# Performance work log

Measured on AMD Instinct MI355X. Metric: run time of the kernel, lower is better.

The kernel has to match this reference:

```python
import jax, jax.numpy as jnp
import numpy as np

B, N, C, H, NL, NH = 8, 1024, 256, 512, 3, 8


def setup_inputs() -> dict:
    key = jax.random.key(0)
    ks = jax.random.split(key, 16)
    g = lambda k, shape: jax.random.normal(k, shape, jnp.float32) * 0.02
    return dict(
        concept_features=jax.random.normal(ks[0], (B, N, C), jnp.float32),
        adjacency_matrix=jax.random.uniform(ks[1], (B, N, N), jnp.float32),
        edge_types=jax.random.randint(ks[2], (B, N, N), 0, 10),
        concept_mask=jnp.ones((B, N), bool),
        W_emb=g(ks[3], (H, C)), b_emb=jnp.zeros((H,), jnp.float32),
        W_in=g(ks[4], (NL, 3 * H, H)), b_in=jnp.zeros((NL, 3 * H), jnp.float32),
        W_out=g(ks[5], (NL, H, H)), b_out=jnp.zeros((NL, H), jnp.float32),
        W_conv=g(ks[6], (NL, H, H)), b_conv=jnp.zeros((NL, H), jnp.float32),
        W_cls=g(ks[7], (1, H)), b_cls=jnp.zeros((1,), jnp.float32),
        W_diff=g(ks[8], (5, H)), b_diff=jnp.zeros((5,), jnp.float32),
        W_pre=g(ks[9], (1, 2 * H)), b_pre=jnp.zeros((1,), jnp.float32),
        W_pool=g(ks[10], (H, H)), b_pool=jnp.zeros((H,), jnp.float32),
    )


def reference(concept_features, adjacency_matrix, edge_types, concept_mask,
              W_emb, b_emb, W_in, b_in, W_out, b_out, W_conv, b_conv,
              W_cls, b_cls, W_diff, b_diff, W_pre, b_pre, W_pool, b_pool):
    Bq, Nc, _ = concept_features.shape
    Hd = W_emb.shape[0]
    dh = Hd // NH

    def mha(x, Wi, bi, Wo, bo):
        # torch nn.MultiheadAttention with batch_first=False: the (B,N,H)
        # input is treated as (seq=B, batch=N, embed=H) -> attention over B.
        qkv = x @ Wi.T + bi                      # (B,N,3H)
        q, k, v = jnp.split(qkv, 3, axis=-1)
        rs = lambda t: t.reshape(Bq, Nc, NH, dh)
        q, k, v = rs(q), rs(k), rs(v)
        sc = jnp.einsum('inhd,jnhd->nhij', q, k) / jnp.sqrt(jnp.float32(dh))
        a = jax.nn.softmax(sc, axis=-1)          # (N,NH,B,B)
        o = jnp.einsum('nhij,jnhd->inhd', a, v).reshape(Bq, Nc, Hd)
        return o @ Wo.T + bo

    def ln(x):  # F.layer_norm, no affine
        m = x.mean(-1, keepdims=True)
        v = ((x - m) ** 2).mean(-1, keepdims=True)
        return (x - m) * jax.lax.rsqrt(v + 1e-5)

    x = concept_features @ W_emb.T + b_emb       # (B,N,H)
    for l in range(W_in.shape[0]):
        att = mha(x, W_in[l], b_in[l], W_out[l], b_out[l])
        conv = att @ W_conv[l].T + b_conv[l]
        agg = jnp.einsum('bij,bjh->bih', adjacency_matrix, conv)
        x = ln(x + agg)

    mastery = x @ W_cls.T + b_cls                # (B,N,1)
    diff = x @ W_diff.T + b_diff                 # (B,N,5)

    # O(N^2) pairwise loop -> bilinear decomposition:
    # score(i,j) = x_i @ W_pre[:, :H].T + x_j @ W_pre[:, H:].T + b
    h1 = (x @ W_pre[:, :Hd].T)[..., 0]           # (B,N)
    h2 = (x @ W_pre[:, Hd:].T)[..., 0]           # (B,N)
    pair = h1[:, :, None] + h2[:, None, :] + b_pre[0]  # (B,N,N)
    off = ~np.eye(Nc, dtype=bool).reshape(-1)    # static mask, i!=j row-major
    prereq = pair.reshape(Bq, Nc * Nc)[:, off][..., None]  # (B,N*(N-1),1)

    graph = x.mean(axis=1) @ W_pool.T + b_pool   # (B,H)
    return (x, mastery, diff, prereq, graph)
```

## Files before the change

kernel.cpp:

```cpp
#include <hip/hip_runtime.h>
#include <hip/hip_bf16.h>

typedef unsigned short ushort_t;
typedef __attribute__((ext_vector_type(4))) float floatx4;
typedef __attribute__((ext_vector_type(8))) __bf16 bf16x8;
typedef __attribute__((ext_vector_type(4))) unsigned short ushortx4;
typedef __attribute__((ext_vector_type(8))) unsigned short ushortx8;

static __device__ __forceinline__ float b2f(ushort_t u) {
  union { unsigned int i; float f; } v; v.i = ((unsigned int)u) << 16; return v.f;
}
static __device__ __forceinline__ ushort_t f2b(float f) {
  unsigned int x = __float_as_uint(f);
  unsigned int r = (x + 0x7fffu + ((x >> 16) & 1u)) >> 16;
  return (ushort_t)r;
}
static __device__ __forceinline__ void glds16(const ushort_t* g, ushort_t* l) {
  __builtin_amdgcn_global_load_lds(
      (const __attribute__((address_space(1))) unsigned int*)g,
      (__attribute__((address_space(3))) unsigned int*)l, 16, 0, 0);
}

template<int MODE, int KS>
__global__ __launch_bounds__(256, 3) void gemm_bt(
    const ushort_t* __restrict__ Ab, const ushort_t* __restrict__ Bm,
    const float* __restrict__ bias,
    ushort_t* __restrict__ C0, ushort_t* __restrict__ C1,
    ushort_t* __restrict__ C2, ushort_t* __restrict__ C3,
    int M, int N, int K, long aBatch, long bBatch, long cBatch)
{
  __shared__ __align__(16) ushort_t As[128 * 64];
  __shared__ __align__(16) ushort_t Bs[128 * 64];

  const int tid  = threadIdx.x;
  const int wid  = tid >> 6;
  const int lane = tid & 63;
  const int quad = lane >> 4;
  const int l16  = lane & 15;
  const int lin = blockIdx.y * gridDim.x + blockIdx.x;
  const int m0 = (lin % gridDim.y) * 128;
  const int n0 = (lin / gridDim.y) * 128;
  const int z  = (KS > 1) ? (int)(blockIdx.z / KS) : blockIdx.z;
  const int kq = (KS > 1) ? (int)(blockIdx.z % KS) : 0;
  const int kbeg = kq * (K / KS);
  const int kend = kbeg + (K / KS);
  ushort_t* outB = C0;
  if (KS >= 2 && kq == 1) outB = C1;
  if (KS >= 4 && kq == 2) outB = C2;
  if (KS >= 4 && kq == 3) outB = C3;

  Ab += (long)z * aBatch;
  Bm += (long)z * bBatch;

  const int wr = (wid >> 1) * 64;
  const int wc = (wid & 1) * 64;

  const int srow = tid >> 3;
  const int scj  = ((tid & 7) ^ (srow & 7)) * 8;
  const long abase = (long)(m0 + srow) * K + scj;
  const long bbase = (long)(n0 + srow) * K + scj;

  floatx4 acc[4][4];
#pragma unroll
  for (int i = 0; i < 4; ++i)
#pragma unroll
    for (int j = 0; j < 4; ++j) acc[i][j] = (floatx4){0.f, 0.f, 0.f, 0.f};

  const int rx = l16 & 7;

  for (int k0 = kbeg; k0 < kend; k0 += 64) {
    __syncthreads();
#pragma unroll
    for (int p = 0; p < 4; ++p)
      glds16(Ab + abase + 32 * p * (long)K + k0, &As[tid * 8 + p * 2048]);
#pragma unroll
    for (int p = 0; p < 4; ++p)
      glds16(Bm + bbase + 32 * p * (long)K + k0, &Bs[tid * 8 + p * 2048]);
    __syncthreads();

#pragma unroll
    for (int kk = 0; kk < 2; ++kk) {
      bf16x8 a[4], b[4];
#pragma unroll
      for (int i = 0; i < 4; ++i)
        a[i] = *(const bf16x8*)(&As[(wr + i * 16 + l16) * 64 +
                                    (((kk * 4 + quad) ^ rx) << 3)]);
#pragma unroll
      for (int j = 0; j < 4; ++j)
        b[j] = *(const bf16x8*)(&Bs[(wc + j * 16 + l16) * 64 +
                                    (((kk * 4 + quad) ^ rx) << 3)]);
#pragma unroll
      for (int i = 0; i < 4; ++i)
#pragma unroll
        for (int j = 0; j < 4; ++j)
          acc[i][j] = __builtin_amdgcn_mfma_f32_16x16x32_bf16(a[i], b[j], acc[i][j], 0, 0, 0);
    }
  }

#pragma unroll
  for (int j = 0; j < 4; ++j) {
    int col = n0 + wc + j * 16 + l16;
    float bv = (bias != nullptr) ? bias[col] : 0.f;
#pragma unroll
    for (int i = 0; i < 4; ++i) {
      int mbase = m0 + wr + i * 16 + quad * 4;
      if constexpr (MODE == 1) {
#pragma unroll
        for (int r = 0; r < 4; ++r)
          outB[(long)z * cBatch + (long)(mbase + r) * N + col] = f2b(acc[i][j][r] + bv);
      } else if constexpr (MODE == 2) {
        int b = mbase >> 10, jrow = mbase & 1023;
        ushortx4 pk;
#pragma unroll
        for (int r = 0; r < 4; ++r) pk[r] = f2b(acc[i][j][r] + bv);
        *(ushortx4*)(outB + ((long)b * N + col) * 1024 + jrow) = pk;
      } else {
        ushort_t* o = (n0 < 512) ? C0 : C1;
        const int cw = (n0 < 512) ? 512 : 1536;
        const int cc = (n0 < 512) ? col : col - 512;
#pragma unroll
        for (int r = 0; r < 4; ++r)
          o[(long)(mbase + r) * cw + cc] = f2b(acc[i][j][r] + bv);
      }
    }
  }
}

__global__ __launch_bounds__(256) void prep_kernel(
    const float* __restrict__ Win,  ushort_t* __restrict__ Winb,
    const float* __restrict__ Wemb, ushort_t* __restrict__ Wq0,
    const float* __restrict__ Wconv, ushort_t* __restrict__ Wcb,
    const float* __restrict__ ADJ,  ushort_t* __restrict__ ADJb,
    const float* __restrict__ CF,   ushort_t* __restrict__ CFb,
    const float* __restrict__ Wout, ushort_t* __restrict__ WoT,
    const float* __restrict__ bout, const float* __restrict__ bconv,
    float* __restrict__ bfused,
    ushort_t* __restrict__ WembT,
    const float* __restrict__ bemb, const float* __restrict__ bin0,
    float* __restrict__ bcat)
{
  __shared__ float tile[64][65];
  const int bid = blockIdx.x, tid = threadIdx.x;
  if (bid < 6720) {
    const float* src; ushort_t* dst; long i;
    if (bid < 1152)      { src = Win;   dst = Winb; i = (long)bid * 256 + tid; }
    else if (bid < 1216) { src = Wemb;  dst = Wq0;  i = (long)(bid - 1152) * 256 + tid; }
    else if (bid < 1600) { src = Wconv; dst = Wcb;  i = (long)(bid - 1216) * 256 + tid; }
    else if (bid < 5696) { src = ADJ;   dst = ADJb; i = (long)(bid - 1600) * 256 + tid; }
    else                 { src = CF;    dst = CFb;  i = (long)(bid - 5696) * 256 + tid; }
    floatx4 a = ((const floatx4*)src)[2 * i];
    floatx4 b = ((const floatx4*)src)[2 * i + 1];
    ushortx4 ha, hb;
#pragma unroll
    for (int r = 0; r < 4; ++r) { ha[r] = f2b(a[r]); hb[r] = f2b(b[r]); }
    ((ushortx4*)dst)[2 * i] = ha; ((ushortx4*)dst)[2 * i + 1] = hb;
  } else if (bid < 6912) {
    const int t = bid - 6720;
    const int z = t >> 6, k0 = ((t >> 3) & 7) * 64, j0 = (t & 7) * 64;
    const long base = (long)z * 262144;
#pragma unroll
    for (int p = 0; p < 16; ++p) {
      int idx = tid + p * 256;
      int jj = idx >> 6, kk = idx & 63;
      tile[jj][kk] = Wout[base + (long)(j0 + jj) * 512 + k0 + kk];
    }
    __syncthreads();
#pragma unroll
    for (int p = 0; p < 16; ++p) {
      int idx = tid + p * 256;
      int kk = idx >> 6, jj = idx & 63;
      WoT[base + (long)(k0 + kk) * 512 + j0 + jj] = f2b(tile[jj][kk]);
    }
  } else if (bid < 6944) {
    const int t = bid - 6912;
    const int j0 = (t >> 2) * 64, k0 = (t & 3) * 64;
#pragma unroll
    for (int p = 0; p < 16; ++p) {
      int idx = tid + p * 256;
      int jj = idx >> 6, kk = idx & 63;
      tile[jj][kk] = Wemb[(long)(j0 + jj) * 256 + k0 + kk];
    }
    __syncthreads();
#pragma unroll
    for (int p = 0; p < 16; ++p) {
      int idx = tid + p * 256;
      int kk = idx >> 6, jj = idx & 63;
      WembT[(long)(k0 + kk) * 512 + j0 + jj] = f2b(tile[jj][kk]);
    }
  } else if (bid < 7328) {
    const int w = tid >> 6, lane = tid & 63;
    const int gi = (bid - 6944) * 4 + w;
    const int l = gi >> 9, o = gi & 511;
    float p = 0.f;
#pragma unroll
    for (int k = 0; k < 8; ++k)
      p += Wconv[(long)l * 262144 + (long)o * 512 + lane + 64 * k] *
           bout[l * 512 + lane + 64 * k];
#pragma unroll
    for (int msk = 1; msk <= 32; msk <<= 1) p += __shfl_xor(p, msk);
    if (lane == 0) bfused[gi] = p + bconv[l * 512 + o];
  } else if (bid < 7712) {
    const int w = tid >> 6, lane = tid & 63;
    const int o = (bid - 7328) * 4 + w;
    float p = 0.f;
#pragma unroll
    for (int k = 0; k < 8; ++k)
      p += Win[(long)o * 512 + lane + 64 * k] * bemb[lane + 64 * k];
#pragma unroll
    for (int msk = 1; msk <= 32; msk <<= 1) p += __shfl_xor(p, msk);
    if (lane == 0) bcat[512 + o] = p + bin0[o];
  } else {
    int idx = (bid - 7712) * 256 + tid;
    bcat[idx] = bemb[idx];
  }
}

__global__ __launch_bounds__(512, 8) void attn_kernel(
    const ushort_t* __restrict__ qkv, ushort_t* __restrict__ outp)
{
  __shared__ ushort_t qs[8 * 1544];
  __shared__ float aw[8][64];
  const int tid = threadIdx.x;
  const int n = blockIdx.x;

  const ushort_t* src = qkv + (long)n * 1536;
#pragma unroll
  for (int p = 0; p < 3; ++p) {
    int c = tid + p * 512;
    int i = c / 192, off = (c % 192) * 8;
    *(ushortx8*)(&qs[i * 1544 + off]) =
        *(const ushortx8*)(src + (long)i * 1024 * 1536 + off);
  }
  __syncthreads();

  const int h    = tid >> 6;
  const int lane = tid & 63;
  const int i = lane >> 3, j = lane & 7;
  const ushort_t* qrow = &qs[i * 1544 + h * 64];
  const ushort_t* krow = &qs[j * 1544 + 512 + h * 64];
  float s = 0.f;
#pragma unroll
  for (int c8 = 0; c8 < 8; ++c8) {
    ushortx8 qa = *(const ushortx8*)(qrow + c8 * 8);
    ushortx8 ka = *(const ushortx8*)(krow + c8 * 8);
#pragma unroll
    for (int r = 0; r < 8; ++r) s += b2f(qa[r]) * b2f(ka[r]);
  }
  s *= 0.125f;

  float m = s;
  m = fmaxf(m, __shfl_xor(m, 1));
  m = fmaxf(m, __shfl_xor(m, 2));
  m = fmaxf(m, __shfl_xor(m, 4));
  float e = __expf(s - m);
  float sum = e;
  sum += __shfl_xor(sum, 1);
  sum += __shfl_xor(sum, 2);
  sum += __shfl_xor(sum, 4);
  aw[h][lane] = e / sum;

  float vv[8];
#pragma unroll
  for (int jj = 0; jj < 8; ++jj)
    vv[jj] = b2f(qs[jj * 1544 + 1024 + h * 64 + lane]);
  const long ob = (long)n * 512 + h * 64 + lane;
#pragma unroll
  for (int ii = 0; ii < 8; ++ii) {
    float acc = 0.f;
#pragma unroll
    for (int jj = 0; jj < 8; ++jj) acc += aw[h][ii * 8 + jj] * vv[jj];
    outp[ob + (long)ii * 1024 * 512] = f2b(acc);
  }
}

__global__ __launch_bounds__(256) void ln_kernel(
    const ushort_t* __restrict__ xb,
    const ushort_t* __restrict__ aggA, const ushort_t* __restrict__ aggB,
    const ushort_t* __restrict__ aggC, const ushort_t* __restrict__ aggD,
    ushort_t* __restrict__ outB)
{
  const int w = threadIdx.x >> 6, lane = threadIdx.x & 63;
  const long base = ((long)blockIdx.x * 4 + w) * 512;
  float v[8];
  float s = 0.f;
#pragma unroll
  for (int k = 0; k < 8; ++k) {
    long idx = base + lane + 64 * k;
    v[k] = b2f(xb[idx]) + b2f(aggA[idx]) + b2f(aggB[idx]) +
           b2f(aggC[idx]) + b2f(aggD[idx]);
    s += v[k];
  }
#pragma unroll
  for (int msk = 1; msk <= 32; msk <<= 1) s += __shfl_xor(s, msk);
  float mean = s * (1.f / 512.f);
  float vv = 0.f;
#pragma unroll
  for (int k = 0; k < 8; ++k) { float d = v[k] - mean; vv += d * d; }
#pragma unroll
  for (int msk = 1; msk <= 32; msk <<= 1) vv += __shfl_xor(vv, msk);
  float inv = rsqrtf(vv * (1.f / 512.f) + 1e-5f);
#pragma unroll
  for (int k = 0; k < 8; ++k)
    outB[base + lane + 64 * k] = f2b((v[k] - mean) * inv);
}

__global__ __launch_bounds__(256) void final_ln_heads_kernel(
    const ushort_t* __restrict__ xb,
    const ushort_t* __restrict__ aggA, const ushort_t* __restrict__ aggB,
    const ushort_t* __restrict__ aggC, const ushort_t* __restrict__ aggD,
    float* __restrict__ out_x,
    const float* __restrict__ Wcls, const float* __restrict__ bcls,
    const float* __restrict__ Wdiff, const float* __restrict__ bdiff,
    const float* __restrict__ Wpre,
    float* __restrict__ mastery, float* __restrict__ diff,
    float* __restrict__ h1, float* __restrict__ h2,
    float* __restrict__ xp)
{
  __shared__ float sp4[4][512];
  const int w = threadIdx.x >> 6, lane = threadIdx.x & 63;
  const long row = (long)blockIdx.x * 4 + w;
  const long base = row * 512;
  float v[8];
  float s = 0.f;
#pragma unroll
  for (int k = 0; k < 8; ++k) {
    long idx = base + lane + 64 * k;
    v[k] = b2f(xb[idx]) + b2f(aggA[idx]) + b2f(aggB[idx]) +
           b2f(aggC[idx]) + b2f(aggD[idx]);
    s += v[k];
  }
#pragma unroll
  for (int msk = 1; msk <= 32; msk <<= 1) s += __shfl_xor(s, msk);
  float mean = s * (1.f / 512.f);
  float vv = 0.f;
#pragma unroll
  for (int k = 0; k < 8; ++k) { float d = v[k] - mean; vv += d * d; }
#pragma unroll
  for (int msk = 1; msk <= 32; msk <<= 1) vv += __shfl_xor(vv, msk);
  float inv = rsqrtf(vv * (1.f / 512.f) + 1e-5f);
#pragma unroll
  for (int k = 0; k < 8; ++k) {
    v[k] = (v[k] - mean) * inv;
    out_x[base + lane + 64 * k] = v[k];
    sp4[w][lane + 64 * k] = v[k];
  }
  __syncthreads();
  for (int t = threadIdx.x; t < 512; t += 256)
    xp[(long)blockIdx.x * 512 + t] =
        sp4[0][t] + sp4[1][t] + sp4[2][t] + sp4[3][t];
#pragma unroll
  for (int o = 0; o < 8; ++o) {
    const float* wp = (o == 0) ? Wcls
                    : (o <= 5) ? (Wdiff + (o - 1) * 512)
                    : (o == 6) ? Wpre : (Wpre + 512);
    float p = 0.f;
#pragma unroll
    for (int k = 0; k < 8; ++k) p += v[k] * wp[lane + 64 * k];
#pragma unroll
    for (int msk = 1; msk <= 32; msk <<= 1) p += __shfl_xor(p, msk);
    if (lane == 0) {
      if (o == 0)      mastery[row] = p + bcls[0];
      else if (o <= 5) diff[row * 5 + (o - 1)] = p + bdiff[o - 1];
      else if (o == 6) h1[row] = p;
      else             h2[row] = p;
    }
  }
}

__global__ __launch_bounds__(256) void epi_kernel(
    const float* __restrict__ h1, const float* __restrict__ h2,
    const float* __restrict__ bpre, float* __restrict__ outp,
    const float* __restrict__ xp, float* __restrict__ xm)
{
  const int bid = blockIdx.x;
  if (bid < 8192) {
    const int b = bid >> 10, i = bid & 1023;
    const float base = h1[b * 1024 + i] + bpre[0];
    const long ob = (long)b * (1024 * 1023) + (long)i * 1023;
#pragma unroll
    for (int r = 0; r < 4; ++r) {
      int j = r * 256 + threadIdx.x;
      if (j == i) continue;
      int pos = (j < i) ? j : j - 1;
      outp[ob + pos] = base + h2[b * 1024 + j];
    }
  } else {
    const int gi = (bid - 8192) * 256 + threadIdx.x;
    const int b = gi >> 9, c = gi & 511;
    const float* p = xp + (long)b * 256 * 512 + c;
    float s = 0.f;
    for (int q = 0; q < 256; ++q) s += p[q * 512];
    xm[b * 512 + c] = s;
  }
}

__global__ __launch_bounds__(256) void graph_kernel(
    const float* __restrict__ xm, const float* __restrict__ Wpool,
    const float* __restrict__ bpool, float* __restrict__ g)
{
  const int gi = blockIdx.x * 256 + threadIdx.x;
  const int b = gi >> 9, o = gi & 511;
  float s = 0.f;
  for (int hh = 0; hh < 512; ++hh) s += xm[b * 512 + hh] * Wpool[o * 512 + hh];
  g[gi] = s * (1.f / 1024.f) + bpool[o];
}

extern "C" void kernel_launch(void* const* d_in, const int* in_sizes, int n_in,
                              void* d_out, int out_size, void* d_ws, size_t ws_size,
                              hipStream_t stream)
{
  const float* CF    = (const float*)d_in[0];
  const float* ADJ   = (const float*)d_in[1];
  const float* Wemb  = (const float*)d_in[4];
  const float* bemb  = (const float*)d_in[5];
  const float* Win   = (const float*)d_in[6];
  const float* bin   = (const float*)d_in[7];
  const float* Wout  = (const float*)d_in[8];
  const float* bout  = (const float*)d_in[9];
  const float* Wconv = (const float*)d_in[10];
  const float* bconv = (const float*)d_in[11];
  const float* Wcls  = (const float*)d_in[12];
  const float* bcls  = (const float*)d_in[13];
  const float* Wdiff = (const float*)d_in[14];
  const float* bdiff = (const float*)d_in[15];
  const float* Wpre  = (const float*)d_in[16];
  const float* bpre  = (const float*)d_in[17];
  const float* Wpool = (const float*)d_in[18];
  const float* bpool = (const float*)d_in[19];

  ushort_t* W = (ushort_t*)d_ws;
  ushort_t* xb   = W;
  ushort_t* qkvb = W + 4194304;
  ushort_t* cT    = qkvb;
  ushort_t* aggA  = qkvb + 4194304;
  ushort_t* aggB  = qkvb + 8388608;
  ushort_t* WoT   = qkvb + 4194304;
  ushort_t* Wcb   = qkvb + 4980736;
  ushort_t* WembT = qkvb + 5767168;
  ushort_t* Winb = W + 16777216;
  ushort_t* Wfb  = W + 19136512;
  ushort_t* ADJb = W + 19922944;
  ushort_t* CFb  = W + 28311552;
  ushort_t* Wq0  = W + 32505856;
  float* bfused = (float*)(W + 33030144);
  float* bcat   = bfused + 1536;
  float* h1     = bcat + 2048;
  float* h2     = h1 + 8192;
  float* xm     = h2 + 8192;
  float* xp     = xm + 4096;

  float* out_x       = (float*)d_out;
  float* out_mastery = out_x + 4194304;
  float* out_diff    = out_mastery + 8192;
  float* out_prereq  = out_diff + 40960;
  float* out_graph   = out_prereq + 8380416;
  ushort_t* aob = (ushort_t*)out_x;
  ushort_t* aggC = (ushort_t*)out_prereq;
  ushort_t* aggD = (ushort_t*)out_prereq + 4194304;

  dim3 blk(256);

  prep_kernel<<<dim3(7714), blk, 0, stream>>>(
      Win, Winb, Wemb, Wq0, Wconv, Wcb, ADJ, ADJb, CF, CFb,
      Wout, WoT, bout, bconv, bfused, WembT, bemb, bin, bcat);
  gemm_bt<1, 1><<<dim3(2, 12, 1), blk, 0, stream>>>(
      Winb, WembT, nullptr, Wq0 + 512 * 256, nullptr, nullptr, nullptr,
      1536, 256, 512, 0, 0, 0);
  gemm_bt<1, 1><<<dim3(4, 4, 3), blk, 0, stream>>>(
      Wcb, WoT, nullptr, Wfb, nullptr, nullptr, nullptr,
      512, 512, 512, 262144, 262144, 262144);

  for (int l = 0; l < 3; ++l) {
    if (l == 0) {
      gemm_bt<3, 1><<<dim3(16, 64, 1), blk, 0, stream>>>(
          CFb, Wq0, bcat, xb, qkvb, nullptr, nullptr,
          8192, 2048, 256, 0, 0, 0);
    } else {
      gemm_bt<1, 1><<<dim3(12, 64, 1), blk, 0, stream>>>(
          xb, Winb + (long)l * 786432, bin + l * 1536,
          qkvb, nullptr, nullptr, nullptr, 8192, 1536, 512, 0, 0, 0);
    }
    attn_kernel<<<dim3(1024), dim3(512), 0, stream>>>(qkvb, aob);
    gemm_bt<2, 1><<<dim3(4, 64, 1), blk, 0, stream>>>(
        aob, Wfb + (long)l * 262144, bfused + l * 512,
        cT, nullptr, nullptr, nullptr, 8192, 512, 512, 0, 0, 0);
    gemm_bt<1, 4><<<dim3(4, 8, 32), blk, 0, stream>>>(
        ADJb, cT, nullptr, aggA, aggB, aggC, aggD,
        1024, 512, 1024, 1048576, 524288, 524288);
    if (l < 2)
      ln_kernel<<<dim3(2048), blk, 0, stream>>>(xb, aggA, aggB, aggC, aggD, xb);
    else
      final_ln_heads_kernel<<<dim3(2048), blk, 0, stream>>>(
          xb, aggA, aggB, aggC, aggD, out_x, Wcls, bcls, Wdiff, bdiff, Wpre,
          out_mastery, out_diff, h1, h2, xp);
  }

  epi_kernel<<<dim3(8208), blk, 0, stream>>>(h1, h2, bpre, out_prereq,
                                             xp, xm);
  graph_kernel<<<dim3(16), blk, 0, stream>>>(xm, Wpool, bpool, out_graph);
}
```

Before: 451.0 us.

## Merge setup GEMMs, halve adjacency split-K, fuse pooling into epilogue kernel

The GEMM body moves into a shared device function so the two weight-precompute GEMMs can run as a single launch. The adjacency aggregation drops from four-way to two-way split-K, so the layer-norm kernels read two partial buffers instead of four. The column-sum and graph-pool kernels are folded into the prereq epilogue, which now writes four rows per block. The aim is fewer kernel launches and less partial-sum traffic, at the cost of fewer blocks (less parallelism) in the aggregation GEMM and a serial per-batch pooling tail.

Measured after the change: 432.9 us. -4.0%, faster.

```diff
diff --git a/kernel.cpp b/kernel.cpp
--- a/kernel.cpp
+++ b/kernel.cpp
@@ -21,22 +21,103 @@
       (__attribute__((address_space(3))) unsigned int*)l, 16, 0, 0);
 }
 
+template<int MODE>
+static __device__ __forceinline__ void gemm_core(
+    const ushort_t* __restrict__ Ab, const ushort_t* __restrict__ Bm,
+    const float* __restrict__ bias,
+    ushort_t* __restrict__ outB, ushort_t* __restrict__ C1,
+    int N, int K, int m0, int n0, int kbeg, int kend,
+    ushort_t* As, ushort_t* Bs)
+{
+  const int tid  = threadIdx.x;
+  const int wid  = tid >> 6;
+  const int lane = tid & 63;
+  const int quad = lane >> 4;
+  const int l16  = lane & 15;
+
+  const int wr = (wid >> 1) * 64;
+  const int wc = (wid & 1) * 64;
+
+  const int srow = tid >> 3;
+  const int scj  = ((tid & 7) ^ (srow & 7)) * 8;
+  const long abase = (long)(m0 + srow) * K + scj;
+  const long bbase = (long)(n0 + srow) * K + scj;
+
+  floatx4 acc[4][4];
+#pragma unroll
+  for (int i = 0; i < 4; ++i)
+#pragma unroll
+    for (int j = 0; j < 4; ++j) acc[i][j] = (floatx4){0.f, 0.f, 0.f, 0.f};
+
+  const int rx = l16 & 7;
+
+  for (int k0 = kbeg; k0 < kend; k0 += 64) {
+    __syncthreads();
+#pragma unroll
+    for (int p = 0; p < 4; ++p)
+      glds16(Ab + abase + 32 * p * (long)K + k0, &As[tid * 8 + p * 2048]);
+#pragma unroll
+    for (int p = 0; p < 4; ++p)
+      glds16(Bm + bbase + 32 * p * (long)K + k0, &Bs[tid * 8 + p * 2048]);
+    __syncthreads();
+
+#pragma unroll
+    for (int kk = 0; kk < 2; ++kk) {
+      bf16x8 a[4], b[4];
+#pragma unroll
+      for (int i = 0; i < 4; ++i)
+        a[i] = *(const bf16x8*)(&As[(wr + i * 16 + l16) * 64 +
+                                    (((kk * 4 + quad) ^ rx) << 3)]);
+#pragma unroll
+      for (int j = 0; j < 4; ++j)
+        b[j] = *(const bf16x8*)(&Bs[(wc + j * 16 + l16) * 64 +
+                                    (((kk * 4 + quad) ^ rx) << 3)]);
+#pragma unroll
+      for (int i = 0; i < 4; ++i)
+#pragma unroll
+        for (int j = 0; j < 4; ++j)
+          acc[i][j] = __builtin_amdgcn_mfma_f32_16x16x32_bf16(a[i], b[j], acc[i][j], 0, 0, 0);
+    }
+  }
+
+#pragma unroll
+  for (int j = 0; j < 4; ++j) {
+    int col = n0 + wc + j * 16 + l16;
+    float bv = (bias != nullptr) ? bias[col] : 0.f;
+#pragma unroll
+    for (int i = 0; i < 4; ++i) {
+      int mbase = m0 + wr + i * 16 + quad * 4;
+      if constexpr (MODE == 1) {
+#pragma unroll
+        for (int r = 0; r < 4; ++r)
+          outB[(long)(mbase + r) * N + col] = f2b(acc[i][j][r] + bv);
+      } else if constexpr (MODE == 2) {
+        int b = mbase >> 10, jrow = mbase & 1023;
+        ushortx4 pk;
+#pragma unroll
+        for (int r = 0; r < 4; ++r) pk[r] = f2b(acc[i][j][r] + bv);
+        *(ushortx4*)(outB + ((long)b * N + col) * 1024 + jrow) = pk;
+      } else {
+        ushort_t* o = (n0 < 512) ? outB : C1;
+        const int cw = (n0 < 512) ? 512 : 1536;
+        const int cc = (n0 < 512) ? col : col - 512;
+#pragma unroll
+        for (int r = 0; r < 4; ++r)
+          o[(long)(mbase + r) * cw + cc] = f2b(acc[i][j][r] + bv);
+      }
+    }
+  }
+}
+
 template<int MODE, int KS>
 __global__ __launch_bounds__(256, 3) void gemm_bt(
     const ushort_t* __restrict__ Ab, const ushort_t* __restrict__ Bm,
     const float* __restrict__ bias,
     ushort_t* __restrict__ C0, ushort_t* __restrict__ C1,
-    ushort_t* __restrict__ C2, ushort_t* __restrict__ C3,
-    int M, int N, int K, long aBatch, long bBatch, long cBatch)
+    int N, int K, long aBatch, long bBatch, long cBatch)
 {
   __shared__ __align__(16) ushort_t As[128 * 64];
   __shared__ __align__(16) ushort_t Bs[128 * 64];
-
-  const int tid  = threadIdx.x;
-  const int wid  = tid >> 6;
-  const int lane = tid & 63;
-  const int quad = lane >> 4;
-  const int l16  = lane & 15;
   const int lin = blockIdx.y * gridDim.x + blockIdx.x;
   const int m0 = (lin % gridDim.y) * 128;
   const int n0 = (lin / gridDim.y) * 128;
@@ -44,85 +125,30 @@
   const int kq = (KS > 1) ? (int)(blockIdx.z % KS) : 0;
   const int kbeg = kq * (K / KS);
   const int kend = kbeg + (K / KS);
-  ushort_t* outB = C0;
-  if (KS >= 2 && kq == 1) outB = C1;
-  if (KS >= 4 && kq == 2) outB = C2;
-  if (KS >= 4 && kq == 3) outB = C3;
-
-  Ab += (long)z * aBatch;
-  Bm += (long)z * bBatch;
-
-  const int wr = (wid >> 1) * 64;
-  const int wc = (wid & 1) * 64;
-
-  const int srow = tid >> 3;
-  const int scj  = ((tid & 7) ^ (srow & 7)) * 8;
-  const long abase = (long)(m0 + srow) * K + scj;
-  const long bbase = (long)(n0 + srow) * K + scj;
-
-  floatx4 acc[4][4];
-#pragma unroll
-  for (int i = 0; i < 4; ++i)
-#pragma unroll
-    for (int j = 0; j < 4; ++j) acc[i][j] = (floatx4){0.f, 0.f, 0.f, 0.f};
-
-  const int rx = l16 & 7;
-
-  for (int k0 = kbeg; k0 < kend; k0 += 64) {
-    __syncthreads();
-#pragma unroll
-    for (int p = 0; p < 4; ++p)
-      glds16(Ab + abase + 32 * p * (long)K + k0, &As[tid * 8 + p * 2048]);
-#pragma unroll
-    for (int p = 0; p < 4; ++p)
-      glds16(Bm + bbase + 32 * p * (long)K + k0, &Bs[tid * 8 + p * 2048]);
-    __syncthreads();
-
-#pragma unroll
-    for (int kk = 0; kk < 2; ++kk) {
-      bf16x8 a[4], b[4];
-#pragma unroll
-      for (int i = 0; i < 4; ++i)
-        a[i] = *(const bf16x8*)(&As[(wr + i * 16 + l16) * 64 +
-                                    (((kk * 4 + quad) ^ rx) << 3)]);
-#pragma unroll
-      for (int j = 0; j < 4; ++j)
-        b[j] = *(const bf16x8*)(&Bs[(wc + j * 16 + l16) * 64 +
-                                    (((kk * 4 + quad) ^ rx) << 3)]);
-#pragma unroll
-      for (int i = 0; i < 4; ++i)
-#pragma unroll
-        for (int j = 0; j < 4; ++j)
-          acc[i][j] = __builtin_amdgcn_mfma_f32_16x16x32_bf16(a[i], b[j], acc[i][j], 0, 0, 0);
-    }
-  }
-
-#pragma unroll
-  for (int j = 0; j < 4; ++j) {
-    int col = n0 + wc + j * 16 + l16;
-    float bv = (bias != nullptr) ? bias[col] : 0.f;
-#pragma unroll
-    for (int i = 0; i < 4; ++i) {
-      int mbase = m0 + wr + i * 16 + quad * 4;
-      if constexpr (MODE == 1) {
-#pragma unroll
-        for (int r = 0; r < 4; ++r)
-          outB[(long)z * cBatch + (long)(mbase + r) * N + col] = f2b(acc[i][j][r] + bv);
-      } else if constexpr (MODE == 2) {
-        int b = mbase >> 10, jrow = mbase & 1023;
-        ushortx4 pk;
-#pragma unroll
-        for (int r = 0; r < 4; ++r) pk[r] = f2b(acc[i][j][r] + bv);
-        *(ushortx4*)(outB + ((long)b * N + col) * 1024 + jrow) = pk;
-      } else {
-        ushort_t* o = (n0 < 512) ? C0 : C1;
-        const int cw = (n0 < 512) ? 512 : 1536;
-        const int cc = (n0 < 512) ? col : col - 512;
-#pragma unroll
-        for (int r = 0; r < 4; ++r)
-          o[(long)(mbase + r) * cw + cc] = f2b(acc[i][j][r] + bv);
-      }
-    }
+  ushort_t* outB = (KS >= 2 && kq == 1) ? C1 : C0;
+  gemm_core<MODE>(Ab + (long)z * aBatch, Bm + (long)z * bBatch, bias,
+                  outB + ((MODE == 1) ? (long)z * cBatch : 0), C1,
+                  N, K, m0, n0, kbeg, kend, As, Bs);
+}
+
+__global__ __launch_bounds__(256, 3) void setup_gemm(
+    const ushort_t* __restrict__ Wcb, const ushort_t* __restrict__ WoT,
+    ushort_t* __restrict__ Wfb,
+    const ushort_t* __restrict__ Winb, const ushort_t* __restrict__ WembT,
+    ushort_t* __restrict__ Wq0t)
+{
+  __shared__ __align__(16) ushort_t As[128 * 64];
+  __shared__ __align__(16) ushort_t Bs[128 * 64];
+  const int lin = blockIdx.x;
+  const int z = blockIdx.z;
+  if (z < 3) {
+    if (lin >= 16) return;
+    const long off = (long)z * 262144;
+    gemm_core<1>(Wcb + off, WoT + off, nullptr, Wfb + off, nullptr,
+                 512, 512, (lin & 3) * 128, (lin >> 2) * 128, 0, 512, As, Bs);
+  } else {
+    gemm_core<1>(Winb, WembT, nullptr, Wq0t, nullptr,
+                 256, 512, (lin % 12) * 128, (lin / 12) * 128, 0, 512, As, Bs);
   }
 }
 
@@ -276,7 +302,6 @@
 __global__ __launch_bounds__(256) void ln_kernel(
     const ushort_t* __restrict__ xb,
     const ushort_t* __restrict__ aggA, const ushort_t* __restrict__ aggB,
-    const ushort_t* __restrict__ aggC, const ushort_t* __restrict__ aggD,
     ushort_t* __restrict__ outB)
 {
   const int w = threadIdx.x >> 6, lane = threadIdx.x & 63;
@@ -286,8 +311,7 @@
 #pragma unroll
   for (int k = 0; k < 8; ++k) {
     long idx = base + lane + 64 * k;
-    v[k] = b2f(xb[idx]) + b2f(aggA[idx]) + b2f(aggB[idx]) +
-           b2f(aggC[idx]) + b2f(aggD[idx]);
+    v[k] = b2f(xb[idx]) + b2f(aggA[idx]) + b2f(aggB[idx]);
     s += v[k];
   }
 #pragma unroll
@@ -307,7 +331,6 @@
 __global__ __launch_bounds__(256) void final_ln_heads_kernel(
     const ushort_t* __restrict__ xb,
     const ushort_t* __restrict__ aggA, const ushort_t* __restrict__ aggB,
-    const ushort_t* __restrict__ aggC, const ushort_t* __restrict__ aggD,
     float* __restrict__ out_x,
     const float* __restrict__ Wcls, const float* __restrict__ bcls,
     const float* __restrict__ Wdiff, const float* __restrict__ bdiff,
@@ -325,8 +348,7 @@
 #pragma unroll
   for (int k = 0; k < 8; ++k) {
     long idx = base + lane + 64 * k;
-    v[k] = b2f(xb[idx]) + b2f(aggA[idx]) + b2f(aggB[idx]) +
-           b2f(aggC[idx]) + b2f(aggD[idx]);
+    v[k] = b2f(xb[idx]) + b2f(aggA[idx]) + b2f(aggB[idx]);
     s += v[k];
   }
 #pragma unroll
@@ -370,39 +392,47 @@
 __global__ __launch_bounds__(256) void epi_kernel(
     const float* __restrict__ h1, const float* __restrict__ h2,
     const float* __restrict__ bpre, float* __restrict__ outp,
-    const float* __restrict__ xp, float* __restrict__ xm)
-{
+    const float* __restrict__ xp, const float* __restrict__ Wpool,
+    const float* __restrict__ bpool, float* __restrict__ g)
+{
+  __shared__ float xms[512];
   const int bid = blockIdx.x;
-  if (bid < 8192) {
-    const int b = bid >> 10, i = bid & 1023;
-    const float base = h1[b * 1024 + i] + bpre[0];
-    const long ob = (long)b * (1024 * 1023) + (long)i * 1023;
-#pragma unroll
-    for (int r = 0; r < 4; ++r) {
-      int j = r * 256 + threadIdx.x;
-      if (j == i) continue;
-      int pos = (j < i) ? j : j - 1;
-      outp[ob + pos] = base + h2[b * 1024 + j];
+  if (bid < 2048) {
+#pragma unroll
+    for (int rr = 0; rr < 4; ++rr) {
+      const int ri = bid * 4 + rr;
+      const int b = ri >> 10, i = ri & 1023;
+      const float base = h1[ri] + bpre[0];
+      const long ob = (long)b * (1024 * 1023) + (long)i * 1023;
+      const float* h2b = h2 + b * 1024;
+#pragma unroll
+      for (int r = 0; r < 4; ++r) {
+        int j = r * 256 + threadIdx.x;
+        if (j == i) continue;
+        int pos = (j < i) ? j : j - 1;
+        outp[ob + pos] = base + h2b[j];
+      }
     }
   } else {
-    const int gi = (bid - 8192) * 256 + threadIdx.x;
-    const int b = gi >> 9, c = gi & 511;
-    const float* p = xp + (long)b * 256 * 512 + c;
-    float s = 0.f;
-    for (int q = 0; q < 256; ++q) s += p[q * 512];
-    xm[b * 512 + c] = s;
-  }
-}
-
-__global__ __launch_bounds__(256) void graph_kernel(
-    const float* __restrict__ xm, const float* __restrict__ Wpool,
-    const float* __restrict__ bpool, float* __restrict__ g)
-{
-  const int gi = blockIdx.x * 256 + threadIdx.x;
-  const int b = gi >> 9, o = gi & 511;
-  float s = 0.f;
-  for (int hh = 0; hh < 512; ++hh) s += xm[b * 512 + hh] * Wpool[o * 512 + hh];
-  g[gi] = s * (1.f / 1024.f) + bpool[o];
+    const int b = bid - 2048;
+    const float* p = xp + (long)b * 256 * 512;
+#pragma unroll
+    for (int cc = 0; cc < 2; ++cc) {
+      int c = threadIdx.x + cc * 256;
+      float s = 0.f;
+      for (int q = 0; q < 256; ++q) s += p[q * 512 + c];
+      xms[c] = s;
+    }
+    __syncthreads();
+#pragma unroll
+    for (int oo = 0; oo < 2; ++oo) {
+      int o = threadIdx.x + oo * 256;
+      const float* wr = Wpool + (long)o * 512;
+      float s = 0.f;
+      for (int hh = 0; hh < 512; ++hh) s += xms[hh] * wr[hh];
+      g[b * 512 + o] = s * (1.f / 1024.f) + bpool[o];
+    }
+  }
 }
 
 extern "C" void kernel_launch(void* const* d_in, const int* in_sizes, int n_in,
@@ -446,8 +476,7 @@
   float* bcat   = bfused + 1536;
   float* h1     = bcat + 2048;
   float* h2     = h1 + 8192;
-  float* xm     = h2 + 8192;
-  float* xp     = xm + 4096;
+  float* xp     = h2 + 8192;
 
   float* out_x       = (float*)d_out;
   float* out_mastery = out_x + 4194304;
@@ -455,47 +484,39 @@
   float* out_prereq  = out_diff + 40960;
   float* out_graph   = out_prereq + 8380416;
   ushort_t* aob = (ushort_t*)out_x;
-  ushort_t* aggC = (ushort_t*)out_prereq;
-  ushort_t* aggD = (ushort_t*)out_prereq + 4194304;
 
   dim3 blk(256);
 
   prep_kernel<<<dim3(7714), blk, 0, stream>>>(
       Win, Winb, Wemb, Wq0, Wconv, Wcb, ADJ, ADJb, CF, CFb,
       Wout, WoT, bout, bconv, bfused, WembT, bemb, bin, bcat);
-  gemm_bt<1, 1><<<dim3(2, 12, 1), blk, 0, stream>>>(
-      Winb, WembT, nullptr, Wq0 + 512 * 256, nullptr, nullptr, nullptr,
-      1536, 256, 512, 0, 0, 0);
-  gemm_bt<1, 1><<<dim3(4, 4, 3), blk, 0, stream>>>(
-      Wcb, WoT, nullptr, Wfb, nullptr, nullptr, nullptr,
-      512, 512, 512, 262144, 262144, 262144);
+  setup_gemm<<<dim3(24, 1, 4), blk, 0, stream>>>(
+      Wcb, WoT, Wfb, Winb, WembT, Wq0 + 512 * 256);
 
   for (int l = 0; l < 3; ++l) {
     if (l == 0) {
       gemm_bt<3, 1><<<dim3(16, 64, 1), blk, 0, stream>>>(
-          CFb, Wq0, bcat, xb, qkvb, nullptr, nullptr,
-          8192, 2048, 256, 0, 0, 0);
+          CFb, Wq0, bcat, xb, qkvb, 2048, 256, 0, 0, 0);
     } else {
       gemm_bt<1, 1><<<dim3(12, 64, 1), blk, 0, stream>>>(
           xb, Winb + (long)l * 786432, bin + l * 1536,
-          qkvb, nullptr, nullptr, nullptr, 8192, 1536, 512, 0, 0, 0);
+          qkvb, nullptr, 1536, 512, 0, 0, 0);
     }
     attn_kernel<<<dim3(1024), dim3(512), 0, stream>>>(qkvb, aob);
     gemm_bt<2, 1><<<dim3(4, 64, 1), blk, 0, stream>>>(
         aob, Wfb + (long)l * 262144, bfused + l * 512,
-        cT, nullptr, nullptr, nullptr, 8192, 512, 512, 0, 0, 0);
-    gemm_bt<1, 4><<<dim3(4, 8, 32), blk, 0, stream>>>(
-        ADJb, cT, nullptr, aggA, aggB, aggC, aggD,
-        1024, 512, 1024, 1048576, 524288, 524288);
+        cT, nullptr, 512, 512, 0, 0, 0);
+    gemm_bt<1, 2><<<dim3(4, 8, 16), blk, 0, stream>>>(
+        ADJb, cT, nullptr, aggA, aggB,
+        512, 1024, 1048576, 524288, 524288);
     if (l < 2)
-      ln_kernel<<<dim3(2048), blk, 0, stream>>>(xb, aggA, aggB, aggC, aggD, xb);
+      ln_kernel<<<dim3(2048), blk, 0, stream>>>(xb, aggA, aggB, xb);
     else
       final_ln_heads_kernel<<<dim3(2048), blk, 0, stream>>>(
-          xb, aggA, aggB, aggC, aggD, out_x, Wcls, bcls, Wdiff, bdiff, Wpre,
+          xb, aggA, aggB, out_x, Wcls, bcls, Wdiff, bdiff, Wpre,
           out_mastery, out_diff, h1, h2, xp);
   }
 
-  epi_kernel<<<dim3(8208), blk, 0, stream>>>(h1, h2, bpre, out_prereq,
-                                             xp, xm);
-  graph_kernel<<<dim3(16), blk, 0, stream>>>(xm, Wpool, bpool, out_graph);
-}
+  epi_kernel<<<dim3(2056), blk, 0, stream>>>(h1, h2, bpre, out_prereq,
+                                             xp, Wpool, bpool, out_graph);
+}
```
